# Performance work log

Hardware: AMD Instinct MI355X
Metric: run time of the kernel (lower is better)

Reference implementation:

```python
import jax, jax.numpy as jnp
import numpy as np

EPS = 1e-6

def _rmsnorm(x, w):
    var = jnp.mean(x * x, axis=-1, keepdims=True)
    return w * (x * jax.lax.rsqrt(var + EPS))

def _rope(t, cos, sin):
    # t: [B,S,H,d_k]; cos/sin: [S,d_k/2] -> complex multiply on (even,odd) pairs
    B, S, H, D = t.shape
    tr = t.reshape(B, S, H, D // 2, 2)
    t0, t1 = tr[..., 0], tr[..., 1]
    c = cos[None, :, None, :]
    s = sin[None, :, None, :]
    o0 = t0 * c - t1 * s
    o1 = t0 * s + t1 * c
    return jnp.stack([o0, o1], axis=-1).reshape(B, S, H, D)

def setup_inputs() -> dict:
    key = jax.random.key(0)
    ks = jax.random.split(key, 9)
    B, S, D, H, DFF = 1, 4096, 1024, 16, 4096
    dk = D // H
    hidden = int(2 * DFF / 3)  # 2730, SwiGLU hidden dim
    sc = 0.02
    x = jax.random.normal(ks[0], (B, S, D), jnp.float32)
    # RoPE tables (theta=10000)
    inv_freq = 1.0 / (10000.0 ** (np.arange(0, dk, 2, dtype=np.float32) / dk))
    ang = np.outer(np.arange(S, dtype=np.float32), inv_freq)
    freqs_cos = jnp.asarray(np.cos(ang))
    freqs_sin = jnp.asarray(np.sin(ang))
    # causal additive mask [1,1,S,S]
    mask = jnp.where(np.tril(np.ones((S, S), bool)), 0.0, -1e9).astype(jnp.float32)[None, None]
    Wq = jax.random.normal(ks[1], (D, D), jnp.float32) * sc
    Wk = jax.random.normal(ks[2], (D, D), jnp.float32) * sc
    Wv = jax.random.normal(ks[3], (D, D), jnp.float32) * sc
    Wo = jax.random.normal(ks[4], (D, D), jnp.float32) * sc
    ln1_w = jnp.ones((D,), jnp.float32)
    ln2_w = jnp.ones((D,), jnp.float32)
    w1 = jax.random.normal(ks[5], (D, hidden), jnp.float32) * sc
    w2 = jax.random.normal(ks[6], (hidden, D), jnp.float32) * sc
    w3 = jax.random.normal(ks[7], (D, hidden), jnp.float32) * sc
    return dict(x=x, freqs_cos=freqs_cos, freqs_sin=freqs_sin, mask=mask,
                Wq=Wq, Wk=Wk, Wv=Wv, Wo=Wo, ln1_w=ln1_w, ln2_w=ln2_w,
                w1=w1, w2=w2, w3=w3)

def reference(x, freqs_cos, freqs_sin, mask, Wq, Wk, Wv, Wo, ln1_w, ln2_w, w1, w2, w3):
    B, S, D = x.shape
    H = 16
    dk = D // H
    scale = jnp.sqrt(jnp.float32(dk))
    # attention sublayer (pre-RMSNorm)
    h = _rmsnorm(x, ln1_w)
    Q = (h @ Wq).reshape(B, S, H, dk)
    K = (h @ Wk).reshape(B, S, H, dk)
    V = (h @ Wv).reshape(B, S, H, dk)
    Q = _rope(Q, freqs_cos, freqs_sin)
    K = _rope(K, freqs_cos, freqs_sin)
    scores = jnp.einsum('bshd,bthd->bhst', Q, K) / scale + mask  # [B,H,S,S]
    attn = jax.nn.softmax(scores, axis=-1)
    ctx = jnp.einsum('bhst,bthd->bshd', attn, V).reshape(B, S, D)
    x = x + ctx @ Wo
    # SwiGLU FFN sublayer
    h2 = _rmsnorm(x, ln2_w)
    ff = (jax.nn.silu(h2 @ w1) * (h2 @ w3)) @ w2
    x = x + ff
    return x
```

## Files before the change

### kernel.cpp

```cpp
#include <hip/hip_runtime.h>

#define S_LEN 4096
#define D_MODEL 1024
#define NHEAD 16
#define DK 64
#define HID 2730
#define HIDP 2880
#define QKV_LD 3072

typedef unsigned short u16;
typedef unsigned int u32;
typedef __bf16 bf16x8 __attribute__((ext_vector_type(8)));
typedef float f32x4 __attribute__((ext_vector_type(4)));

#define MFMA16 __builtin_amdgcn_mfma_f32_16x16x32_bf16
#define EXP2 __builtin_amdgcn_exp2f

__device__ __forceinline__ float b2f(u16 u) {
    return __builtin_bit_cast(float, (u32)u << 16);
}
__device__ __forceinline__ u16 f2b(float f) {
    u32 u = __builtin_bit_cast(u32, f);
    u += 0x7FFF + ((u >> 16) & 1);
    return (u16)(u >> 16);
}
__device__ __forceinline__ u32 pk_trunc(float lo, float hi) {
    return __builtin_amdgcn_perm(__builtin_bit_cast(u32, hi),
                                 __builtin_bit_cast(u32, lo), 0x07060302u);
}
__device__ __forceinline__ void gll16(const u16* g, u16* l) {
    __builtin_amdgcn_global_load_lds(
        (__attribute__((address_space(1))) void*)(g),
        (__attribute__((address_space(3))) void*)(l),
        16, 0, 0);
}

__global__ __launch_bounds__(256)
void prep_k(const float* s0, const float* s1, const float* s2,
            const float* s3, const float* s4, const float* s5,
            const float* s6, u16* d0, u16* d1, u16* d2, u16* d3,
            u16* d4, u16* d5, u16* d6,
            const float* __restrict__ x, const float* __restrict__ ln1,
            u16* __restrict__ hb) {
    __shared__ float t[32][33];
    __shared__ float red[4];
    const int bid = blockIdx.x;
    const int tid = threadIdx.x;

    if (bid >= 12736) {
        const int row = bid - 12736;
        const float4 v = ((const float4*)(x + (size_t)row * D_MODEL))[tid];
        float ss = v.x * v.x + v.y * v.y + v.z * v.z + v.w * v.w;
        for (int o = 32; o; o >>= 1) ss += __shfl_down(ss, o);
        if ((tid & 63) == 0) red[tid >> 6] = ss;
        __syncthreads();
        const float tot = red[0] + red[1] + red[2] + red[3];
        const float rs = rsqrtf(tot * (1.0f / D_MODEL) + 1e-6f);
        const float4 wv = ((const float4*)ln1)[tid];
        u16* op = hb + (size_t)row * D_MODEL + tid * 4;
        u32 p0 = (u32)f2b(v.x * rs * wv.x) | ((u32)f2b(v.y * rs * wv.y) << 16);
        u32 p1 = (u32)f2b(v.z * rs * wv.z) | ((u32)f2b(v.w * rs * wv.w) << 16);
        uint2 pk; pk.x = p0; pk.y = p1;
        *(uint2*)op = pk;
        return;
    }

    const float* srcs[7] = {s0, s1, s2, s3, s4, s5, s6};
    u16* dsts[7] = {d0, d1, d2, d3, d4, d5, d6};
    const int RR[7] = {1024, 1024, 1024, 1024, 1024, 1024, 2730};
    const int CC[7] = {1024, 1024, 1024, 1024, 2730, 2730, 1024};
    const int OC[7] = {1024, 1024, 1024, 1024, 1024, 1024, 2880};
    const int XD[7] = {32, 32, 32, 32, 32, 32, 90};

    int seg, start;
    if (bid < 4096)      { seg = bid >> 10; start = seg << 10; }
    else if (bid < 6976) { seg = 4; start = 4096; }
    else if (bid < 9856) { seg = 5; start = 6976; }
    else                 { seg = 6; start = 9856; }
    const int local = bid - start;
    const int bx = local % XD[seg], byy = local / XD[seg];
    const float* in = srcs[seg];
    u16* out = dsts[seg];
    const int R = RR[seg], C = CC[seg], outC = OC[seg];

    const int r0 = byy * 32;
    const int c0 = bx * 32;
    const int tx = tid & 31, ty = tid >> 5;
#pragma unroll
    for (int j = 0; j < 4; ++j) {
        int ir = c0 + ty + j * 8;
        int ic = r0 + tx;
        t[ty + j * 8][tx] = (ir < R && ic < C) ? in[(size_t)ir * C + ic] : 0.0f;
    }
    __syncthreads();
#pragma unroll
    for (int j = 0; j < 4; ++j)
        out[(size_t)(r0 + ty + j * 8) * outC + c0 + tx] = f2b(t[tx][ty + j * 8]);
}

__global__ __launch_bounds__(256)
void rmsnorm_k(const float* __restrict__ x, const float* __restrict__ w,
               u16* __restrict__ out) {
    const int row = blockIdx.x;
    const int tid = threadIdx.x;
    const float4 v = ((const float4*)(x + (size_t)row * D_MODEL))[tid];
    float ss = v.x * v.x + v.y * v.y + v.z * v.z + v.w * v.w;
    for (int o = 32; o; o >>= 1) ss += __shfl_down(ss, o);
    __shared__ float red[4];
    if ((tid & 63) == 0) red[tid >> 6] = ss;
    __syncthreads();
    const float tot = red[0] + red[1] + red[2] + red[3];
    const float rs = rsqrtf(tot * (1.0f / D_MODEL) + 1e-6f);
    const float4 wv = ((const float4*)w)[tid];
    u16* op = out + (size_t)row * D_MODEL + tid * 4;
    u32 p0 = (u32)f2b(v.x * rs * wv.x) | ((u32)f2b(v.y * rs * wv.y) << 16);
    u32 p1 = (u32)f2b(v.z * rs * wv.z) | ((u32)f2b(v.w * rs * wv.w) << 16);
    uint2 pk; pk.x = p0; pk.y = p1;
    *(uint2*)op = pk;
}

__global__ __launch_bounds__(256)
void packkv_k(const u16* __restrict__ qkv, const float* __restrict__ fc,
              const float* __restrict__ fs, u16* __restrict__ vt,
              u16* __restrict__ kp) {
    __shared__ u16 t[32][33];
    const int h = blockIdx.z;
    const int t0 = blockIdx.x * 32;
    const int d0 = blockIdx.y * 32;
    const int tx = threadIdx.x, ty = threadIdx.y;
#pragma unroll
    for (int j = 0; j < 4; ++j)
        t[ty + j * 8][tx] =
            qkv[(size_t)(t0 + ty + j * 8) * QKV_LD + 2 * D_MODEL + h * DK + d0 + tx];

    const int id = ty * 32 + tx;
    const int sA = t0 + (id >> 3);
    const int dA = d0 + (id & 7) * 4;
    uint2 kvp = *(const uint2*)(qkv + (size_t)sA * QKV_LD + D_MODEL + h * DK + dA);
    const int fi = sA * 32 + (dA >> 1);
    const float cc0 = fc[fi], ss0 = fs[fi];
    const float cc1 = fc[fi + 1], ss1 = fs[fi + 1];
    auto rpk = [](u32 w, float c, float s) -> u32 {
        const float a = b2f((u16)w), b = b2f((u16)(w >> 16));
        return (u32)f2b(a * c - b * s) | ((u32)f2b(a * s + b * c) << 16);
    };
    kvp.x = rpk(kvp.x, cc0, ss0);
    kvp.y = rpk(kvp.y, cc1, ss1);
    *(uint2*)(kp + ((size_t)h * S_LEN + sA) * DK + dA) = kvp;

    __syncthreads();
#pragma unroll
    for (int j = 0; j < 4; ++j)
        vt[(size_t)h * DK * S_LEN + (size_t)(d0 + ty + j * 8) * S_LEN + t0 + tx] =
            t[tx][ty + j * 8];
}

template <int EPI>
__global__ __launch_bounds__(256)
void gemm128(const u16* __restrict__ A, int lda, const u16* __restrict__ Bt, int ldb,
             void* __restrict__ C, int ldc, int K, const float* __restrict__ resid) {
    const int m0 = blockIdx.y * 128, n0 = blockIdx.x * 128;
    const int tid = threadIdx.x;
    const int wave = tid >> 6, lane = tid & 63;
    const int wr = wave >> 1, wc = wave & 1;
    const int r16 = lane & 15, kq = lane >> 4;

    __shared__ __align__(16) u16 As[128 * 32];
    __shared__ __align__(16) u16 Bs[128 * 32];

    const int srow = tid >> 2, sk = (tid & 3) * 8;
    const u16* ag0 = A + (size_t)(m0 + srow) * lda + sk;
    const u16* ag1 = A + (size_t)(m0 + 64 + srow) * lda + sk;
    const u16* bg0 = Bt + (size_t)(n0 + srow) * ldb + sk;
    const u16* bg1 = Bt + (size_t)(n0 + 64 + srow) * ldb + sk;
    u16* asw = As + wave * 512;
    u16* bsw = Bs + wave * 512;

    f32x4 acc[16];
#pragma unroll
    for (int i = 0; i < 16; ++i) acc[i] = f32x4{0.f, 0.f, 0.f, 0.f};

    for (int k0 = 0; k0 < K; k0 += 32) {
        __syncthreads();
        gll16(ag0 + k0, asw);
        gll16(ag1 + k0, asw + 2048);
        gll16(bg0 + k0, bsw);
        gll16(bg1 + k0, bsw + 2048);
        __syncthreads();
        bf16x8 af[4], bf[4];
#pragma unroll
        for (int mt = 0; mt < 4; ++mt)
            af[mt] = *(const bf16x8*)&As[(wr * 64 + mt * 16 + r16) * 32 + kq * 8];
#pragma unroll
        for (int nt = 0; nt < 4; ++nt)
            bf[nt] = *(const bf16x8*)&Bs[(wc * 64 + nt * 16 + r16) * 32 + kq * 8];
#pragma unroll
        for (int mt = 0; mt < 4; ++mt)
#pragma unroll
            for (int nt = 0; nt < 4; ++nt)
                acc[mt * 4 + nt] = MFMA16(af[mt], bf[nt], acc[mt * 4 + nt], 0, 0, 0);
    }

#pragma unroll
    for (int mt = 0; mt < 4; ++mt) {
#pragma unroll
        for (int nt = 0; nt < 4; ++nt) {
            const int col = n0 + wc * 64 + nt * 16 + r16;
#pragma unroll
            for (int j = 0; j < 4; ++j) {
                const int row = m0 + wr * 64 + mt * 16 + kq * 4 + j;
                if (EPI == 0) {
                    ((u16*)C)[(size_t)row * ldc + col] = f2b(acc[mt * 4 + nt][j]);
                } else {
                    ((float*)C)[(size_t)row * ldc + col] =
                        resid[(size_t)row * ldc + col] + acc[mt * 4 + nt][j];
                }
            }
        }
    }
}

__global__ __launch_bounds__(256)
void gemm64r(const u16* __restrict__ A, int lda, const u16* __restrict__ Bt, int ldb,
             float* __restrict__ C, int ldc, int K, const float* __restrict__ resid) {
    const int m0 = blockIdx.y * 128, n0 = blockIdx.x * 64;
    const int tid = threadIdx.x;
    const int wave = tid >> 6, lane = tid & 63;
    const int r16 = lane & 15, kq = lane >> 4;

    __shared__ __align__(16) u16 As[128 * 32];
    __shared__ __align__(16) u16 Bs[64 * 32];

    const int srow = tid >> 2, sk = (tid & 3) * 8;
    const u16* ag0 = A + (size_t)(m0 + srow) * lda + sk;
    const u16* ag1 = A + (size_t)(m0 + 64 + srow) * lda + sk;
    const u16* bg = Bt + (size_t)(n0 + srow) * ldb + sk;
    u16* asw = As + wave * 512;
    u16* bsw = Bs + wave * 512;

    f32x4 acc[8];
#pragma unroll
    for (int i = 0; i < 8; ++i) acc[i] = f32x4{0.f, 0.f, 0.f, 0.f};

    for (int k0 = 0; k0 < K; k0 += 32) {
        __syncthreads();
        gll16(ag0 + k0, asw);
        gll16(ag1 + k0, asw + 2048);
        gll16(bg + k0, bsw);
        __syncthreads();
        bf16x8 af[2], bf[4];
#pragma unroll
        for (int mt = 0; mt < 2; ++mt)
            af[mt] = *(const bf16x8*)&As[(wave * 32 + mt * 16 + r16) * 32 + kq * 8];
#pragma unroll
        for (int nt = 0; nt < 4; ++nt)
            bf[nt] = *(const bf16x8*)&Bs[(nt * 16 + r16) * 32 + kq * 8];
#pragma unroll
        for (int mt = 0; mt < 2; ++mt)
#pragma unroll
            for (int nt = 0; nt < 4; ++nt)
                acc[mt * 4 + nt] = MFMA16(af[mt], bf[nt], acc[mt * 4 + nt], 0, 0, 0);
    }

#pragma unroll
    for (int mt = 0; mt < 2; ++mt)
#pragma unroll
        for (int nt = 0; nt < 4; ++nt) {
            const int col = n0 + nt * 16 + r16;
#pragma unroll
            for (int j = 0; j < 4; ++j) {
                const int row = m0 + wave * 32 + mt * 16 + kq * 4 + j;
                C[(size_t)row * ldc + col] =
                    resid[(size_t)row * ldc + col] + acc[mt * 4 + nt][j];
            }
        }
}

__global__ __launch_bounds__(256, 3)
void gemm_dual96x(const u16* __restrict__ A, int lda,
                  const u16* __restrict__ B1, const u16* __restrict__ B3, int ldb,
                  u16* __restrict__ C, int ldc, int K) {
    const int m0 = blockIdx.y * 128, n0 = blockIdx.x * 96;
    const int tid = threadIdx.x;
    const int wave = tid >> 6, lane = tid & 63;
    const int wr = wave >> 1, wc = wave & 1;
    const int r16 = lane & 15, kq = lane >> 4;

    __shared__ __align__(16) u16 As[128 * 64];
    __shared__ __align__(16) u16 Bs[192 * 64];

    const int srow = tid >> 3;
    const int scol = ((tid & 7) ^ (srow & 7)) * 8;
    const u16* ag0 = A + (size_t)(m0 +  0 + srow) * lda + scol;
    const u16* ag1 = A + (size_t)(m0 + 32 + srow) * lda + scol;
    const u16* ag2 = A + (size_t)(m0 + 64 + srow) * lda + scol;
    const u16* ag3 = A + (size_t)(m0 + 96 + srow) * lda + scol;
    const u16* bg0 = B1 + (size_t)(n0 +  0 + srow) * ldb + scol;
    const u16* bg1 = B1 + (size_t)(n0 + 32 + srow) * ldb + scol;
    const u16* bg2 = B1 + (size_t)(n0 + 64 + srow) * ldb + scol;
    const u16* bg3 = B3 + (size_t)(n0 +  0 + srow) * ldb + scol;
    const u16* bg4 = B3 + (size_t)(n0 + 32 + srow) * ldb + scol;
    const u16* bg5 = B3 + (size_t)(n0 + 64 + srow) * ldb + scol;
    u16* const ad = As + tid * 8;
    u16* const bd = Bs + tid * 8;

    f32x4 acc1[12], acc3[12];
#pragma unroll
    for (int i = 0; i < 12; ++i) {
        acc1[i] = f32x4{0.f, 0.f, 0.f, 0.f};
        acc3[i] = f32x4{0.f, 0.f, 0.f, 0.f};
    }

    const int rsw = r16 & 7;
    for (int k0 = 0; k0 < K; k0 += 64) {
        __syncthreads();
        gll16(ag0 + k0, ad);
        gll16(ag1 + k0, ad + 2048);
        gll16(ag2 + k0, ad + 4096);
        gll16(ag3 + k0, ad + 6144);
        gll16(bg0 + k0, bd);
        gll16(bg1 + k0, bd + 2048);
        gll16(bg2 + k0, bd + 4096);
        gll16(bg3 + k0, bd + 6144);
        gll16(bg4 + k0, bd + 8192);
        gll16(bg5 + k0, bd + 10240);
        __syncthreads();
#pragma unroll
        for (int ks = 0; ks < 2; ++ks) {
            const int slot = (((ks << 2) | kq) ^ rsw) * 8;
            bf16x8 af[4], b1f[3], b3f[3];
#pragma unroll
            for (int mt = 0; mt < 4; ++mt)
                af[mt] = *(const bf16x8*)&As[(wr * 64 + mt * 16 + r16) * 64 + slot];
#pragma unroll
            for (int nt = 0; nt < 3; ++nt) {
                b1f[nt] = *(const bf16x8*)&Bs[(wc * 48 + nt * 16 + r16) * 64 + slot];
                b3f[nt] = *(const bf16x8*)&Bs[(96 + wc * 48 + nt * 16 + r16) * 64 + slot];
            }
#pragma unroll
            for (int mt = 0; mt < 4; ++mt)
#pragma unroll
                for (int nt = 0; nt < 3; ++nt) {
                    acc1[mt * 3 + nt] = MFMA16(af[mt], b1f[nt], acc1[mt * 3 + nt], 0, 0, 0);
                    acc3[mt * 3 + nt] = MFMA16(af[mt], b3f[nt], acc3[mt * 3 + nt], 0, 0, 0);
                }
        }
    }

#pragma unroll
    for (int mt = 0; mt < 4; ++mt)
#pragma unroll
        for (int nt = 0; nt < 3; ++nt) {
            const int col = n0 + wc * 48 + nt * 16 + r16;
#pragma unroll
            for (int j = 0; j < 4; ++j) {
                const int row = m0 + wr * 64 + mt * 16 + kq * 4 + j;
                const float v1 = acc1[mt * 3 + nt][j];
                const float v3 = acc3[mt * 3 + nt][j];
                const float sig = 1.0f / (1.0f + __expf(-v1));
                C[(size_t)row * ldc + col] = f2b(v1 * sig * v3);
            }
        }
}

__global__ __launch_bounds__(256)
void flash_k(const u16* __restrict__ qkv, const u16* __restrict__ vt,
             const u16* __restrict__ kp, const float* __restrict__ fc,
             const float* __restrict__ fs, u16* __restrict__ ctx) {
    const int h = blockIdx.x;
    const int pair = blockIdx.y;
    const int qa = pair, qb = 63 - pair;
    const int tid = threadIdx.x;
    const int wave = tid >> 6, lane = tid & 63;
    const int r16 = lane & 15, kq = lane >> 4;

    __shared__ __align__(16) u16 Kb[2][64 * 64];
    __shared__ __align__(16) u16 Vb[2][64 * 64];
    __shared__ __align__(16) u16 Ps[4 * 16 * 64];

    const u16* kb = kp + (size_t)h * S_LEN * DK;
    const u16* vb = vt + (size_t)h * DK * S_LEN;
    const int srow = tid >> 3;
    const int lcol = ((tid & 7) ^ (srow & 7)) * 8;
    const int qloc = wave * 16 + r16;
    const int sw = r16 & 7;
    const int c0 = (kq ^ sw) * 8;
    const int c1 = ((4 ^ kq) ^ sw) * 8;
    const int psw = r16 & 14;
    u16* psrow = Ps + wave * 1024 + r16 * 64;

    const float SC = 0.125f * 1.44269504f;
    auto rp = [SC](u32 w, float c, float s) -> u32 {
        const float a = b2f((u16)w), b = b2f((u16)(w >> 16));
        return (u32)f2b((a * c - b * s) * SC) |
               ((u32)f2b((a * s + b * c) * SC) << 16);
    };
    auto loadq = [&](int qglob, bf16x8& q0out, bf16x8& q1out) {
        const u16* qrow = qkv + (size_t)qglob * QKV_LD + h * DK;
        uint4 uq0 = *(const uint4*)(qrow + kq * 8);
        uint4 uq1 = *(const uint4*)(qrow + 32 + kq * 8);
        const float4 c0v = *(const float4*)(fc + qglob * 32 + kq * 4);
        const float4 s0v = *(const float4*)(fs + qglob * 32 + kq * 4);
        const float4 c1v = *(const float4*)(fc + qglob * 32 + 16 + kq * 4);
        const float4 s1v = *(const float4*)(fs + qglob * 32 + 16 + kq * 4);
        uq0.x = rp(uq0.x, c0v.x, s0v.x); uq0.y = rp(uq0.y, c0v.y, s0v.y);
        uq0.z = rp(uq0.z, c0v.z, s0v.z); uq0.w = rp(uq0.w, c0v.w, s0v.w);
        uq1.x = rp(uq1.x, c1v.x, s1v.x); uq1.y = rp(uq1.y, c1v.y, s1v.y);
        uq1.z = rp(uq1.z, c1v.z, s1v.z); uq1.w = rp(uq1.w, c1v.w, s1v.w);
        q0out = __builtin_bit_cast(bf16x8, uq0);
        q1out = __builtin_bit_cast(bf16x8, uq1);
    };
    const int qgA = qa * 64 + qloc;
    const int qgB = qb * 64 + qloc;
    bf16x8 qfA0, qfA1, qfB0, qfB1;
    loadq(qgA, qfA0, qfA1);
    loadq(qgB, qfB0, qfB1);

    f32x4 oA[4], oB[4];
#pragma unroll
    for (int i = 0; i < 4; ++i) {
        oA[i] = f32x4{0.f, 0.f, 0.f, 0.f};
        oB[i] = f32x4{0.f, 0.f, 0.f, 0.f};
    }
    f32x4 laccA = f32x4{0.f, 0.f, 0.f, 0.f};
    f32x4 laccB = f32x4{0.f, 0.f, 0.f, 0.f};
    const uint4 uone = make_uint4(0x3F803F80u, 0x3F803F80u, 0x3F803F80u, 0x3F803F80u);
    const bf16x8 ones = __builtin_bit_cast(bf16x8, uone);

    auto tilec = [&](const u16* Ks, const u16* Vs, const bf16x8& q0f,
                     const bf16x8& q1f, f32x4 (&o)[4], f32x4& lacc, bool dmask) {
        f32x4 s[4];
#pragma unroll
        for (int nt = 0; nt < 4; ++nt) {
            s[nt] = f32x4{0.f, 0.f, 0.f, 0.f};
            const bf16x8 k0 = *(const bf16x8*)&Ks[(nt * 16 + r16) * 64 + c0];
            s[nt] = MFMA16(k0, q0f, s[nt], 0, 0, 0);
            const bf16x8 k1 = *(const bf16x8*)&Ks[(nt * 16 + r16) * 64 + c1];
            s[nt] = MFMA16(k1, q1f, s[nt], 0, 0, 0);
        }
        float pr[16];
#pragma unroll
        for (int nt = 0; nt < 4; ++nt)
#pragma unroll
            for (int j = 0; j < 4; ++j) pr[nt * 4 + j] = EXP2(s[nt][j]);
        if (dmask) {
#pragma unroll
            for (int nt = 0; nt < 4; ++nt)
#pragma unroll
                for (int j = 0; j < 4; ++j)
                    if ((nt * 16 + kq * 4 + j) > qloc) pr[nt * 4 + j] = 0.f;
        }
#pragma unroll
        for (int nt = 0; nt < 4; ++nt) {
            uint2 pk;
            pk.x = pk_trunc(pr[nt * 4 + 0], pr[nt * 4 + 1]);
            pk.y = pk_trunc(pr[nt * 4 + 2], pr[nt * 4 + 3]);
            *(uint2*)&psrow[((nt * 4 + kq) ^ psw) * 4] = pk;
        }
#pragma unroll
        for (int ks = 0; ks < 2; ++ks) {
            const bf16x8 pf = *(const bf16x8*)&psrow[((8 * ks + 2 * kq) ^ psw) * 4];
            lacc = MFMA16(ones, pf, lacc, 0, 0, 0);
            const int cv = (((ks << 2) ^ kq) ^ sw) * 8;
#pragma unroll
            for (int nt = 0; nt < 4; ++nt) {
                const bf16x8 vf = *(const bf16x8*)&Vs[(nt * 16 + r16) * 64 + cv];
                o[nt] = MFMA16(vf, pf, o[nt], 0, 0, 0);
            }
        }
    };

#pragma unroll
    for (int i = 0; i < 2; ++i) {
        const int r = srow + i * 32;
        gll16(kb + (size_t)r * DK + lcol, Kb[0] + tid * 8 + i * 2048);
        gll16(vb + (size_t)r * S_LEN + lcol, Vb[0] + tid * 8 + i * 2048);
    }

    for (int t = 0; t <= qb; ++t) {
        __syncthreads();
        if (t < qb) {
            const int t1 = (t + 1) * 64;
            u16* kd = Kb[(t + 1) & 1];
            u16* vd = Vb[(t + 1) & 1];
#pragma unroll
            for (int i = 0; i < 2; ++i) {
                const int r = srow + i * 32;
                gll16(kb + (size_t)(t1 + r) * DK + lcol, kd + tid * 8 + i * 2048);
                gll16(vb + (size_t)r * S_LEN + t1 + lcol, vd + tid * 8 + i * 2048);
            }
        }
        const u16* Ks = Kb[t & 1];
        const u16* Vs = Vb[t & 1];

        tilec(Ks, Vs, qfB0, qfB1, oB, laccB, t == qb);
        if (t <= qa)
            tilec(Ks, Vs, qfA0, qfA1, oA, laccA, t == qa);
    }

    auto wout = [&](f32x4 (&o)[4], float lsum, int qg) {
        const float inv = 1.0f / lsum;
        const size_t row = qg;
#pragma unroll
        for (int nt = 0; nt < 4; ++nt) {
            uint2 pk;
            pk.x = (u32)f2b(o[nt][0] * inv) | ((u32)f2b(o[nt][1] * inv) << 16);
            pk.y = (u32)f2b(o[nt][2] * inv) | ((u32)f2b(o[nt][3] * inv) << 16);
            *(uint2*)&ctx[row * D_MODEL + h * DK + nt * 16 + kq * 4] = pk;
        }
    };
    wout(oA, laccA[0], qgA);
    wout(oB, laccB[0], qgB);
}

extern "C" void kernel_launch(void* const* d_in, const int* in_sizes, int n_in,
                              void* d_out, int out_size, void* d_ws, size_t ws_size,
                              hipStream_t stream) {
    const float* x    = (const float*)d_in[0];
    const float* fcos = (const float*)d_in[1];
    const float* fsin = (const float*)d_in[2];
    const float* Wq = (const float*)d_in[4];
    const float* Wk = (const float*)d_in[5];
    const float* Wv = (const float*)d_in[6];
    const float* Wo = (const float*)d_in[7];
    const float* ln1 = (const float*)d_in[8];
    const float* ln2 = (const float*)d_in[9];
    const float* w1 = (const float*)d_in[10];
    const float* w2 = (const float*)d_in[11];
    const float* w3 = (const float*)d_in[12];
    float* out = (float*)d_out;

    char* ws = (char*)d_ws;
    size_t off = 0;
    auto alloc = [&](size_t bytes) -> char* {
        char* p = ws + off;
        off += (bytes + 255) & ~(size_t)255;
        return p;
    };
    u16* hb    = (u16*)alloc((size_t)S_LEN * D_MODEL * 2);
    u16* wqkvt = (u16*)alloc((size_t)QKV_LD * D_MODEL * 2);
    u16* wot   = (u16*)alloc((size_t)D_MODEL * D_MODEL * 2);
    u16* qkvb  = (u16*)alloc((size_t)S_LEN * QKV_LD * 2);
    u16* vt    = (u16*)alloc((size_t)S_LEN * D_MODEL * 2);
    u16* kpack = (u16*)alloc((size_t)S_LEN * D_MODEL * 2);
    u16* ctxb  = (u16*)alloc((size_t)S_LEN * D_MODEL * 2);
    float* x2  = (float*)alloc((size_t)S_LEN * D_MODEL * 4);
    u16* h2b   = (u16*)alloc((size_t)S_LEN * D_MODEL * 2);
    u16* w1t   = (u16*)alloc((size_t)HIDP * D_MODEL * 2);
    u16* w3t   = (u16*)alloc((size_t)HIDP * D_MODEL * 2);
    u16* w2t   = (u16*)alloc((size_t)D_MODEL * HIDP * 2);
    u16* ffb   = (u16*)alloc((size_t)S_LEN * HIDP * 2);

    const dim3 tb32(32, 8);

    prep_k<<<16832, 256, 0, stream>>>(
        Wq, Wk, Wv, Wo, w1, w3, w2,
        wqkvt, wqkvt + (size_t)D_MODEL * D_MODEL,
        wqkvt + (size_t)2 * D_MODEL * D_MODEL, wot, w1t, w3t, w2t,
        x, ln1, hb);

    gemm128<0><<<dim3(QKV_LD / 128, S_LEN / 128), 256, 0, stream>>>(
        hb, D_MODEL, wqkvt, D_MODEL, qkvb, QKV_LD, D_MODEL, nullptr);

    packkv_k<<<dim3(S_LEN / 32, DK / 32, NHEAD), tb32, 0, stream>>>(
        qkvb, fcos, fsin, vt, kpack);

    flash_k<<<dim3(NHEAD, 32), 256, 0, stream>>>(qkvb, vt, kpack, fcos, fsin, ctxb);

    gemm64r<<<dim3(D_MODEL / 64, S_LEN / 128), 256, 0, stream>>>(
        ctxb, D_MODEL, wot, D_MODEL, x2, D_MODEL, D_MODEL, x);

    rmsnorm_k<<<S_LEN, 256, 0, stream>>>(x2, ln2, h2b);

    gemm_dual96x<<<dim3(HIDP / 96, S_LEN / 128), 256, 0, stream>>>(
        h2b, D_MODEL, w1t, w3t, D_MODEL, ffb, HIDP, D_MODEL);

    gemm64r<<<dim3(D_MODEL / 64, S_LEN / 128), 256, 0, stream>>>(
        ffb, HIDP, w2t, HIDP, out, D_MODEL, HIDP, x2);
}
```

Baseline: 427.3 us.

## Split flash attention KV range across two blocks and combine partials

The causal attention kernel gains a third grid dimension. Each query-tile pair is now processed by two blocks. One handles the short query tile plus the first half of the long tile's keys; the other handles the second half of the long tile's keys. Unnormalized partial outputs and row sums for the long tile go to fp32 workspace, and a new combine kernel adds them and writes bf16 context. The aim is to double the number of blocks and halve the per-block serial work, improving CU occupancy and latency hiding. The cost is an extra launch and fp32 partial traffic.

```diff
diff --git a/kernel.cpp b/kernel.cpp
--- a/kernel.cpp
+++ b/kernel.cpp
@@ -366,10 +366,12 @@
 __global__ __launch_bounds__(256)
 void flash_k(const u16* __restrict__ qkv, const u16* __restrict__ vt,
              const u16* __restrict__ kp, const float* __restrict__ fc,
-             const float* __restrict__ fs, u16* __restrict__ ctx) {
+             const float* __restrict__ fs, u16* __restrict__ ctx,
+             float* __restrict__ po, float* __restrict__ pl) {
     const int h = blockIdx.x;
-    const int pair = blockIdx.y;
-    const int qa = pair, qb = 63 - pair;
+    const int p = blockIdx.y;
+    const int sid = blockIdx.z;
+    const int qa = p, qb = 63 - p;
     const int tid = threadIdx.x;
     const int wave = tid >> 6, lane = tid & 63;
     const int r16 = lane & 15, kq = lane >> 4;
@@ -410,20 +412,7 @@
         q0out = __builtin_bit_cast(bf16x8, uq0);
         q1out = __builtin_bit_cast(bf16x8, uq1);
     };
-    const int qgA = qa * 64 + qloc;
-    const int qgB = qb * 64 + qloc;
-    bf16x8 qfA0, qfA1, qfB0, qfB1;
-    loadq(qgA, qfA0, qfA1);
-    loadq(qgB, qfB0, qfB1);
-
-    f32x4 oA[4], oB[4];
-#pragma unroll
-    for (int i = 0; i < 4; ++i) {
-        oA[i] = f32x4{0.f, 0.f, 0.f, 0.f};
-        oB[i] = f32x4{0.f, 0.f, 0.f, 0.f};
-    }
-    f32x4 laccA = f32x4{0.f, 0.f, 0.f, 0.f};
-    f32x4 laccB = f32x4{0.f, 0.f, 0.f, 0.f};
+
     const uint4 uone = make_uint4(0x3F803F80u, 0x3F803F80u, 0x3F803F80u, 0x3F803F80u);
     const bf16x8 ones = __builtin_bit_cast(bf16x8, uone);
 
@@ -470,47 +459,146 @@
         }
     };
 
-#pragma unroll
-    for (int i = 0; i < 2; ++i) {
-        const int r = srow + i * 32;
-        gll16(kb + (size_t)r * DK + lcol, Kb[0] + tid * 8 + i * 2048);
-        gll16(vb + (size_t)r * S_LEN + lcol, Vb[0] + tid * 8 + i * 2048);
-    }
-
-    for (int t = 0; t <= qb; ++t) {
-        __syncthreads();
-        if (t < qb) {
-            const int t1 = (t + 1) * 64;
-            u16* kd = Kb[(t + 1) & 1];
-            u16* vd = Vb[(t + 1) & 1];
+    float* const pob = po + ((size_t)(h * 32 + p) * 2 + sid) * 4096 + tid * 16;
+    float* const plb = pl + ((size_t)(h * 32 + p) * 2 + sid) * 256 + tid;
+
+    if (sid == 0) {
+        const int qgA = qa * 64 + qloc;
+        const int qgB = qb * 64 + qloc;
+        bf16x8 qfA0, qfA1, qfB0, qfB1;
+        loadq(qgA, qfA0, qfA1);
+        loadq(qgB, qfB0, qfB1);
+
+        f32x4 oA[4], oB[4];
+#pragma unroll
+        for (int i = 0; i < 4; ++i) {
+            oA[i] = f32x4{0.f, 0.f, 0.f, 0.f};
+            oB[i] = f32x4{0.f, 0.f, 0.f, 0.f};
+        }
+        f32x4 laccA = f32x4{0.f, 0.f, 0.f, 0.f};
+        f32x4 laccB = f32x4{0.f, 0.f, 0.f, 0.f};
+
+        const int tbB = 31 - p;
+        const int tmax = (p > tbB) ? p : tbB;
+
+#pragma unroll
+        for (int i = 0; i < 2; ++i) {
+            const int r = srow + i * 32;
+            gll16(kb + (size_t)r * DK + lcol, Kb[0] + tid * 8 + i * 2048);
+            gll16(vb + (size_t)r * S_LEN + lcol, Vb[0] + tid * 8 + i * 2048);
+        }
+
+        for (int t = 0; t <= tmax; ++t) {
+            __syncthreads();
+            if (t < tmax) {
+                const int t1 = (t + 1) * 64;
+                u16* kd = Kb[(t + 1) & 1];
+                u16* vd = Vb[(t + 1) & 1];
+#pragma unroll
+                for (int i = 0; i < 2; ++i) {
+                    const int r = srow + i * 32;
+                    gll16(kb + (size_t)(t1 + r) * DK + lcol, kd + tid * 8 + i * 2048);
+                    gll16(vb + (size_t)r * S_LEN + t1 + lcol, vd + tid * 8 + i * 2048);
+                }
+            }
+            const u16* Ks = Kb[t & 1];
+            const u16* Vs = Vb[t & 1];
+            if (t <= tbB) tilec(Ks, Vs, qfB0, qfB1, oB, laccB, false);
+            if (t <= qa)  tilec(Ks, Vs, qfA0, qfA1, oA, laccA, t == qa);
+        }
+
+        {
+            const float inv = 1.0f / laccA[0];
+            const size_t row = qgA;
+#pragma unroll
+            for (int nt = 0; nt < 4; ++nt) {
+                uint2 pk;
+                pk.x = (u32)f2b(oA[nt][0] * inv) | ((u32)f2b(oA[nt][1] * inv) << 16);
+                pk.y = (u32)f2b(oA[nt][2] * inv) | ((u32)f2b(oA[nt][3] * inv) << 16);
+                *(uint2*)&ctx[row * D_MODEL + h * DK + nt * 16 + kq * 4] = pk;
+            }
+        }
+#pragma unroll
+        for (int nt = 0; nt < 4; ++nt) {
+            float4 v;
+            v.x = oB[nt][0]; v.y = oB[nt][1]; v.z = oB[nt][2]; v.w = oB[nt][3];
+            *(float4*)&pob[nt * 4] = v;
+        }
+        *plb = laccB[0];
+    } else {
+        const int qgB = qb * 64 + qloc;
+        bf16x8 qfB0, qfB1;
+        loadq(qgB, qfB0, qfB1);
+
+        f32x4 oB[4];
+#pragma unroll
+        for (int i = 0; i < 4; ++i) oB[i] = f32x4{0.f, 0.f, 0.f, 0.f};
+        f32x4 laccB = f32x4{0.f, 0.f, 0.f, 0.f};
+
+        const int t1s = 32 - p;
+
+        {
+            const int tb = t1s * 64;
 #pragma unroll
             for (int i = 0; i < 2; ++i) {
                 const int r = srow + i * 32;
-                gll16(kb + (size_t)(t1 + r) * DK + lcol, kd + tid * 8 + i * 2048);
-                gll16(vb + (size_t)r * S_LEN + t1 + lcol, vd + tid * 8 + i * 2048);
-            }
-        }
-        const u16* Ks = Kb[t & 1];
-        const u16* Vs = Vb[t & 1];
-
-        tilec(Ks, Vs, qfB0, qfB1, oB, laccB, t == qb);
-        if (t <= qa)
-            tilec(Ks, Vs, qfA0, qfA1, oA, laccA, t == qa);
-    }
-
-    auto wout = [&](f32x4 (&o)[4], float lsum, int qg) {
-        const float inv = 1.0f / lsum;
-        const size_t row = qg;
+                gll16(kb + (size_t)(tb + r) * DK + lcol, Kb[0] + tid * 8 + i * 2048);
+                gll16(vb + (size_t)r * S_LEN + tb + lcol, Vb[0] + tid * 8 + i * 2048);
+            }
+        }
+
+        for (int i = 0; i < 32; ++i) {
+            __syncthreads();
+            if (i < 31) {
+                const int t1 = (t1s + i + 1) * 64;
+                u16* kd = Kb[(i + 1) & 1];
+                u16* vd = Vb[(i + 1) & 1];
+#pragma unroll
+                for (int j = 0; j < 2; ++j) {
+                    const int r = srow + j * 32;
+                    gll16(kb + (size_t)(t1 + r) * DK + lcol, kd + tid * 8 + j * 2048);
+                    gll16(vb + (size_t)r * S_LEN + t1 + lcol, vd + tid * 8 + j * 2048);
+                }
+            }
+            const u16* Ks = Kb[i & 1];
+            const u16* Vs = Vb[i & 1];
+            tilec(Ks, Vs, qfB0, qfB1, oB, laccB, i == 31);
+        }
+
 #pragma unroll
         for (int nt = 0; nt < 4; ++nt) {
-            uint2 pk;
-            pk.x = (u32)f2b(o[nt][0] * inv) | ((u32)f2b(o[nt][1] * inv) << 16);
-            pk.y = (u32)f2b(o[nt][2] * inv) | ((u32)f2b(o[nt][3] * inv) << 16);
-            *(uint2*)&ctx[row * D_MODEL + h * DK + nt * 16 + kq * 4] = pk;
-        }
-    };
-    wout(oA, laccA[0], qgA);
-    wout(oB, laccB[0], qgB);
+            float4 v;
+            v.x = oB[nt][0]; v.y = oB[nt][1]; v.z = oB[nt][2]; v.w = oB[nt][3];
+            *(float4*)&pob[nt * 4] = v;
+        }
+        *plb = laccB[0];
+    }
+}
+
+__global__ __launch_bounds__(256)
+void fcomb_k(const float* __restrict__ po, const float* __restrict__ pl,
+             u16* __restrict__ ctx) {
+    const int hp = blockIdx.x;
+    const int h = hp >> 5, p = hp & 31;
+    const int tid = threadIdx.x;
+    const int wave = tid >> 6, lane = tid & 63;
+    const int r16 = lane & 15, kq = lane >> 4;
+
+    const float l = pl[(size_t)hp * 512 + tid] + pl[(size_t)hp * 512 + 256 + tid];
+    const float inv = 1.0f / l;
+    const float* o0 = po + (size_t)hp * 8192 + tid * 16;
+    const float* o1 = o0 + 4096;
+    const size_t row = (size_t)(63 - p) * 64 + wave * 16 + r16;
+
+#pragma unroll
+    for (int nt = 0; nt < 4; ++nt) {
+        const float4 a = *(const float4*)&o0[nt * 4];
+        const float4 b = *(const float4*)&o1[nt * 4];
+        uint2 pk;
+        pk.x = (u32)f2b((a.x + b.x) * inv) | ((u32)f2b((a.y + b.y) * inv) << 16);
+        pk.y = (u32)f2b((a.z + b.z) * inv) | ((u32)f2b((a.w + b.w) * inv) << 16);
+        *(uint2*)&ctx[row * D_MODEL + h * DK + nt * 16 + kq * 4] = pk;
+    }
 }
 
 extern "C" void kernel_launch(void* const* d_in, const int* in_sizes, int n_in,
@@ -550,6 +638,8 @@
     u16* w3t   = (u16*)alloc((size_t)HIDP * D_MODEL * 2);
     u16* w2t   = (u16*)alloc((size_t)D_MODEL * HIDP * 2);
     u16* ffb   = (u16*)alloc((size_t)S_LEN * HIDP * 2);
+    float* po  = (float*)alloc((size_t)512 * 8192 * 4);
+    float* pl  = (float*)alloc((size_t)512 * 512 * 4);
 
     const dim3 tb32(32, 8);
 
@@ -565,7 +655,10 @@
     packkv_k<<<dim3(S_LEN / 32, DK / 32, NHEAD), tb32, 0, stream>>>(
         qkvb, fcos, fsin, vt, kpack);
 
-    flash_k<<<dim3(NHEAD, 32), 256, 0, stream>>>(qkvb, vt, kpack, fcos, fsin, ctxb);
+    flash_k<<<dim3(NHEAD, 32, 2), 256, 0, stream>>>(
+        qkvb, vt, kpack, fcos, fsin, ctxb, po, pl);
+
+    fcomb_k<<<512, 256, 0, stream>>>(po, pl, ctxb);
 
     gemm64r<<<dim3(D_MODEL / 64, S_LEN / 128), 256, 0, stream>>>(
         ctxb, D_MODEL, wot, D_MODEL, x2, D_MODEL, D_MODEL, x);
```

New measurement: 426.1 us. No clear change (-0.3%).

## Double K-tile depth to 64 with XOR-swizzled LDS layout in gemm128 and gemm64r

Applied to the files above, without the earlier changes.

Both bf16 GEMM kernels now stage a 64-wide K slice per iteration instead of 32, which halves the number of barrier pairs per K, and run two MFMA sub-steps per stage. The LDS layout uses an XOR swizzle of the 16-byte column chunk by row, applied through the global-load-to-LDS address and the fragment reads, to avoid bank conflicts on the wider 128-byte rows. Shared memory per block doubles, which may reduce occupancy, and K must be a multiple of 64.

```diff
diff --git a/kernel.cpp b/kernel.cpp
--- a/kernel.cpp
+++ b/kernel.cpp
@@ -165,40 +165,54 @@
     const int wr = wave >> 1, wc = wave & 1;
     const int r16 = lane & 15, kq = lane >> 4;
 
-    __shared__ __align__(16) u16 As[128 * 32];
-    __shared__ __align__(16) u16 Bs[128 * 32];
-
-    const int srow = tid >> 2, sk = (tid & 3) * 8;
-    const u16* ag0 = A + (size_t)(m0 + srow) * lda + sk;
-    const u16* ag1 = A + (size_t)(m0 + 64 + srow) * lda + sk;
-    const u16* bg0 = Bt + (size_t)(n0 + srow) * ldb + sk;
-    const u16* bg1 = Bt + (size_t)(n0 + 64 + srow) * ldb + sk;
-    u16* asw = As + wave * 512;
-    u16* bsw = Bs + wave * 512;
+    __shared__ __align__(16) u16 As[128 * 64];
+    __shared__ __align__(16) u16 Bs[128 * 64];
+
+    const int srow = tid >> 3;
+    const int scol = ((tid & 7) ^ (srow & 7)) * 8;
+    const u16* ag0 = A + (size_t)(m0 +  0 + srow) * lda + scol;
+    const u16* ag1 = A + (size_t)(m0 + 32 + srow) * lda + scol;
+    const u16* ag2 = A + (size_t)(m0 + 64 + srow) * lda + scol;
+    const u16* ag3 = A + (size_t)(m0 + 96 + srow) * lda + scol;
+    const u16* bg0 = Bt + (size_t)(n0 +  0 + srow) * ldb + scol;
+    const u16* bg1 = Bt + (size_t)(n0 + 32 + srow) * ldb + scol;
+    const u16* bg2 = Bt + (size_t)(n0 + 64 + srow) * ldb + scol;
+    const u16* bg3 = Bt + (size_t)(n0 + 96 + srow) * ldb + scol;
+    u16* const ad = As + tid * 8;
+    u16* const bd = Bs + tid * 8;
 
     f32x4 acc[16];
 #pragma unroll
     for (int i = 0; i < 16; ++i) acc[i] = f32x4{0.f, 0.f, 0.f, 0.f};
 
-    for (int k0 = 0; k0 < K; k0 += 32) {
-        __syncthreads();
-        gll16(ag0 + k0, asw);
-        gll16(ag1 + k0, asw + 2048);
-        gll16(bg0 + k0, bsw);
-        gll16(bg1 + k0, bsw + 2048);
-        __syncthreads();
-        bf16x8 af[4], bf[4];
-#pragma unroll
-        for (int mt = 0; mt < 4; ++mt)
-            af[mt] = *(const bf16x8*)&As[(wr * 64 + mt * 16 + r16) * 32 + kq * 8];
-#pragma unroll
-        for (int nt = 0; nt < 4; ++nt)
-            bf[nt] = *(const bf16x8*)&Bs[(wc * 64 + nt * 16 + r16) * 32 + kq * 8];
-#pragma unroll
-        for (int mt = 0; mt < 4; ++mt)
+    const int rsw = r16 & 7;
+    for (int k0 = 0; k0 < K; k0 += 64) {
+        __syncthreads();
+        gll16(ag0 + k0, ad);
+        gll16(ag1 + k0, ad + 2048);
+        gll16(ag2 + k0, ad + 4096);
+        gll16(ag3 + k0, ad + 6144);
+        gll16(bg0 + k0, bd);
+        gll16(bg1 + k0, bd + 2048);
+        gll16(bg2 + k0, bd + 4096);
+        gll16(bg3 + k0, bd + 6144);
+        __syncthreads();
+#pragma unroll
+        for (int ks = 0; ks < 2; ++ks) {
+            const int slot = (((ks << 2) | kq) ^ rsw) * 8;
+            bf16x8 af[4], bf[4];
+#pragma unroll
+            for (int mt = 0; mt < 4; ++mt)
+                af[mt] = *(const bf16x8*)&As[(wr * 64 + mt * 16 + r16) * 64 + slot];
 #pragma unroll
             for (int nt = 0; nt < 4; ++nt)
-                acc[mt * 4 + nt] = MFMA16(af[mt], bf[nt], acc[mt * 4 + nt], 0, 0, 0);
+                bf[nt] = *(const bf16x8*)&Bs[(wc * 64 + nt * 16 + r16) * 64 + slot];
+#pragma unroll
+            for (int mt = 0; mt < 4; ++mt)
+#pragma unroll
+                for (int nt = 0; nt < 4; ++nt)
+                    acc[mt * 4 + nt] = MFMA16(af[mt], bf[nt], acc[mt * 4 + nt], 0, 0, 0);
+        }
     }
 
 #pragma unroll
@@ -228,38 +242,50 @@
     const int wave = tid >> 6, lane = tid & 63;
     const int r16 = lane & 15, kq = lane >> 4;
 
-    __shared__ __align__(16) u16 As[128 * 32];
-    __shared__ __align__(16) u16 Bs[64 * 32];
-
-    const int srow = tid >> 2, sk = (tid & 3) * 8;
-    const u16* ag0 = A + (size_t)(m0 + srow) * lda + sk;
-    const u16* ag1 = A + (size_t)(m0 + 64 + srow) * lda + sk;
-    const u16* bg = Bt + (size_t)(n0 + srow) * ldb + sk;
-    u16* asw = As + wave * 512;
-    u16* bsw = Bs + wave * 512;
+    __shared__ __align__(16) u16 As[128 * 64];
+    __shared__ __align__(16) u16 Bs[64 * 64];
+
+    const int srow = tid >> 3;
+    const int scol = ((tid & 7) ^ (srow & 7)) * 8;
+    const u16* ag0 = A + (size_t)(m0 +  0 + srow) * lda + scol;
+    const u16* ag1 = A + (size_t)(m0 + 32 + srow) * lda + scol;
+    const u16* ag2 = A + (size_t)(m0 + 64 + srow) * lda + scol;
+    const u16* ag3 = A + (size_t)(m0 + 96 + srow) * lda + scol;
+    const u16* bg0 = Bt + (size_t)(n0 +  0 + srow) * ldb + scol;
+    const u16* bg1 = Bt + (size_t)(n0 + 32 + srow) * ldb + scol;
+    u16* const ad = As + tid * 8;
+    u16* const bd = Bs + tid * 8;
 
     f32x4 acc[8];
 #pragma unroll
     for (int i = 0; i < 8; ++i) acc[i] = f32x4{0.f, 0.f, 0.f, 0.f};
 
-    for (int k0 = 0; k0 < K; k0 += 32) {
-        __syncthreads();
-        gll16(ag0 + k0, asw);
-        gll16(ag1 + k0, asw + 2048);
-        gll16(bg + k0, bsw);
-        __syncthreads();
-        bf16x8 af[2], bf[4];
-#pragma unroll
-        for (int mt = 0; mt < 2; ++mt)
-            af[mt] = *(const bf16x8*)&As[(wave * 32 + mt * 16 + r16) * 32 + kq * 8];
-#pragma unroll
-        for (int nt = 0; nt < 4; ++nt)
-            bf[nt] = *(const bf16x8*)&Bs[(nt * 16 + r16) * 32 + kq * 8];
-#pragma unroll
-        for (int mt = 0; mt < 2; ++mt)
+    const int rsw = r16 & 7;
+    for (int k0 = 0; k0 < K; k0 += 64) {
+        __syncthreads();
+        gll16(ag0 + k0, ad);
+        gll16(ag1 + k0, ad + 2048);
+        gll16(ag2 + k0, ad + 4096);
+        gll16(ag3 + k0, ad + 6144);
+        gll16(bg0 + k0, bd);
+        gll16(bg1 + k0, bd + 2048);
+        __syncthreads();
+#pragma unroll
+        for (int ks = 0; ks < 2; ++ks) {
+            const int slot = (((ks << 2) | kq) ^ rsw) * 8;
+            bf16x8 af[2], bf[4];
+#pragma unroll
+            for (int mt = 0; mt < 2; ++mt)
+                af[mt] = *(const bf16x8*)&As[(wave * 32 + mt * 16 + r16) * 64 + slot];
 #pragma unroll
             for (int nt = 0; nt < 4; ++nt)
-                acc[mt * 4 + nt] = MFMA16(af[mt], bf[nt], acc[mt * 4 + nt], 0, 0, 0);
+                bf[nt] = *(const bf16x8*)&Bs[(nt * 16 + r16) * 64 + slot];
+#pragma unroll
+            for (int mt = 0; mt < 2; ++mt)
+#pragma unroll
+                for (int nt = 0; nt < 4; ++nt)
+                    acc[mt * 4 + nt] = MFMA16(af[mt], bf[nt], acc[mt * 4 + nt], 0, 0, 0);
+        }
     }
 
 #pragma unroll
```

Result: faster. 381.9 us (-10.6%).
